# Kernel tuning notes

Hardware: AMD Instinct MI355X
Metric: run time of the kernel (lower is better)

The kernel has to match this reference:

```python
import jax, jax.numpy as jnp
import numpy as np

ANGLE_SCALE = 100.0
DIST_SCALE = 100.0
DIST_BOUNDARY = 0.0
HID = 128
N_HIDDEN = 2  # output_layer
EPS = 1e-08


def _mlp(x, w0, b0, ws, bs):
    # Linear, then N_HIDDEN x (ReLU, Linear)
    h = x @ w0 + b0
    for i in range(ws.shape[0]):
        h = jax.nn.relu(h) @ ws[i] + bs[i]
    return h


def _capsule_endpoints(x):
    # x: [..., 9] -> A, B endpoints of capsule segment, radius r
    c, s = jnp.cos(x[..., 3:4] * ANGLE_SCALE), jnp.sin(x[..., 3:4] * ANGLE_SCALE)
    half = x[..., 2:3] / 2
    ctr = x[..., 0:2]
    off = jnp.concatenate([half * c, half * s], axis=-1)
    return ctr - off, ctr + off, x[..., 4:5]


def _pt_seg_dist(P, A, AB, AB_sq):
    t = jnp.clip(((P - A) * AB).sum(-1, keepdims=True) / AB_sq, 0.0, 1.0)
    Q = A + t * AB
    return jnp.linalg.norm(P - Q, axis=-1, keepdims=True)


def _dist_to_capsule(init_e, query_e):
    A1, B1, r1 = _capsule_endpoints(init_e)
    A2, B2, r2 = _capsule_endpoints(query_e)
    A1B1, A2B2 = B1 - A1, B2 - A2
    s1 = (A1B1 ** 2).sum(-1, keepdims=True) + EPS
    s2 = (A2B2 ** 2).sum(-1, keepdims=True) + EPS
    d = jnp.minimum(
        jnp.minimum(_pt_seg_dist(A2, A1, A1B1, s1), _pt_seg_dist(B2, A1, A1B1, s1)),
        jnp.minimum(_pt_seg_dist(A1, A2, A2B2, s2), _pt_seg_dist(B1, A2, A2B2, s2)),
    )
    return d - r1 - r2


def setup_inputs() -> dict:
    key = jax.random.key(0)
    ks = jax.random.split(key, 32)
    B, O, T = 64, 64, 64
    f = lambda k, shp, scale=1.0: jax.random.normal(k, shp, dtype=jnp.float32) * scale
    inp = {
        'init_x': f(ks[0], (B, O, 9)),
        'query_x': f(ks[1], (B, T, 9)),
        'init_v': f(ks[2], (B, O, 2)),
        'query_v': f(ks[3], (B, T, 2)),
        'init_angular_v': f(ks[4], (B, O, 1)),
        'query_angular_v': f(ks[5], (B, T, 1)),
        'trunk_w0': f(ks[6], (9, HID), 0.3), 'trunk_b0': f(ks[7], (HID,), 0.1),
        'trunk_ws': f(ks[8], (N_HIDDEN, HID, HID), 0.08), 'trunk_bs': f(ks[9], (N_HIDDEN, HID), 0.1),
        'branch_w0': f(ks[10], (5, HID), 0.3), 'branch_b0': f(ks[11], (HID,), 0.1),
        'branch_ws': f(ks[12], (N_HIDDEN, HID, HID), 0.08), 'branch_bs': f(ks[13], (N_HIDDEN, HID), 0.1),
        'out_w': f(ks[14], (HID, 3), 0.08), 'out_b': f(ks[15], (3,), 0.1),
        'spring_w0': f(ks[16], (1, HID), 0.3), 'spring_b0': f(ks[17], (HID,), 0.1),
        'spring_w1': f(ks[18], (HID, 1), 0.08), 'spring_b1': f(ks[19], (1,), 0.1),
        'joint_w0': f(ks[20], (15, HID), 0.3), 'joint_b0': f(ks[21], (HID,), 0.1),
        'joint_w1': f(ks[22], (HID, 2), 0.08), 'joint_b1': f(ks[23], (2,), 0.1),
    }
    return inp


def reference(init_x, query_x, init_v, query_v, init_angular_v, query_angular_v,
              trunk_w0, trunk_b0, trunk_ws, trunk_bs,
              branch_w0, branch_b0, branch_ws, branch_bs,
              out_w, out_b, spring_w0, spring_b0, spring_w1, spring_b1,
              joint_w0, joint_b0, joint_w1, joint_b1):
    B, O, _ = init_x.shape
    T = query_x.shape[1]
    # pairwise broadcast: init along obj axis (dim1), query along target axis (dim2)
    init_e = jnp.broadcast_to(init_x[:, :, None, :], (B, O, T, 9))
    query_e = jnp.broadcast_to(query_x[:, None, :, :], (B, O, T, 9))
    rel = query_e[..., :2] - init_e[..., :2]
    query_e = jnp.concatenate([rel, query_e[..., 2:]], axis=-1)
    init_e = jnp.concatenate([jnp.zeros_like(rel), init_e[..., 2:]], axis=-1)
    qv = query_v[:, None, :, :] - init_v[:, :, None, :]           # [B,O,T,2]
    qav = query_angular_v[:, None, :, :] - init_angular_v[:, :, None, :]  # [B,O,T,1]
    iav = jnp.broadcast_to(init_angular_v[:, :, None, :], (B, O, T, 1))

    dist = _dist_to_capsule(init_e, query_e)
    dist_mask = (dist <= DIST_BOUNDARY).astype(jnp.float32)
    dist_input = dist * dist_mask * DIST_SCALE

    branch_in = init_e[..., :5]
    trunk_in = jnp.concatenate([query_e[..., :5], qv, qav, dist_input], axis=-1)
    branch_out = _mlp(branch_in, branch_w0, branch_b0, branch_ws, branch_bs)
    trunk_out = _mlp(trunk_in, trunk_w0, trunk_b0, trunk_ws, trunk_bs)
    force = (branch_out * trunk_out) @ out_w + out_b  # [B,O,T,3]

    # spring force
    have_spring = ((init_e[..., 8:9] == query_e[..., 8:9]) & (init_e[..., 8:9] > 0)).astype(jnp.float32)
    dvec = init_e[..., :2] - query_e[..., :2]
    length = jnp.linalg.norm(dvec, axis=-1, keepdims=True)
    dvec = dvec / (length + EPS)
    sf = jax.nn.relu(length @ spring_w0 + spring_b0) @ spring_w1 + spring_b1  # [B,O,T,1]
    sf = sf * dvec
    sf = jnp.concatenate([sf, jnp.zeros_like(sf[..., :1])], axis=-1) * have_spring

    # joint force (torch .long() truncates toward zero)
    i7, q7 = init_e[..., 7:8], query_e[..., 7:8]
    have_joint = ((jnp.trunc(i7) == jnp.trunc(q7)) & (i7 > 0)).astype(jnp.float32)
    joint_in = jnp.concatenate([init_e[..., :5], query_e[..., :5], qv, iav, qav, i7 - jnp.trunc(i7)], axis=-1)
    jf = jax.nn.relu(joint_in @ joint_w0 + joint_b0) @ joint_w1 + joint_b1  # [B,O,T,2]
    jf = jf * have_joint
    jf = jnp.concatenate([jf, jnp.zeros_like(jf[..., :1])], axis=-1)

    force = force * dist_mask + sf + jf
    return force
```

## Files before the change

kernel.cpp:

```cpp
#include <hip/hip_runtime.h>
#include <math.h>


typedef _Float16 h4v __attribute__((ext_vector_type(4)));
typedef _Float16 h8v __attribute__((ext_vector_type(8)));
typedef float    f4v __attribute__((ext_vector_type(4)));

#define AH 136

#define TW0_OFF 0
#define JW0_OFF 4096
#define TWS_OFF 8192
#define BW0_OFF 40960
#define BWS_OFF 45056
#define W_TOTAL 77824
#define BR_OFF_F (W_TOTAL/2)

#define H_ACTA 0
#define H_ACTB 8704
#define H_TINB 8704
#define H_JINB 10752
#define SMH_SIZE 17408

#define F_SCAL  0
#define SMF_SIZE 384

#define FRAG_BLOCKS 304
#define BR_BLOCKS   256

__global__ __launch_bounds__(256)
void prep_kernel(const float* __restrict__ tw0, const float* __restrict__ tws,
                 const float* __restrict__ jw0, const float* __restrict__ bw0,
                 const float* __restrict__ bws, const float* __restrict__ bb0,
                 const float* __restrict__ bbs, const float* __restrict__ init_x,
                 _Float16* __restrict__ wsH, float* __restrict__ brw)
{
    __shared__ float bsm[2*16*132];
    const int tid = threadIdx.x;

    if (blockIdx.x < FRAG_BLOCKS) {
        int idx = blockIdx.x * 256 + tid;
        if (idx >= W_TOTAL) return;
        const int j = idx & 7;
        const int lane = (idx >> 3) & 63;
        const int q = lane >> 4, r = lane & 15;
        _Float16 v;
        if (idx < JW0_OFF) {
            int mt = idx >> 9;
            int k = q*8 + j, m = mt*16 + r;
            v = (k < 9) ? (_Float16)tw0[k*128 + m] : (_Float16)0.f;
        } else if (idx < TWS_OFF) {
            int mt = (idx - JW0_OFF) >> 9;
            int k = q*8 + j, m = mt*16 + r;
            v = (k < 15) ? (_Float16)jw0[k*128 + m] : (_Float16)0.f;
        } else if (idx < BW0_OFF) {
            int e = idx - TWS_OFF;
            int ks = (e >> 9) & 3, mt = (e >> 11) & 7, l = e >> 14;
            int k = ks*32 + q*8 + j, m = mt*16 + r;
            v = (_Float16)tws[l*16384 + k*128 + m];
        } else if (idx < BWS_OFF) {
            int mt = (idx - BW0_OFF) >> 9;
            int k = q*8 + j, m = mt*16 + r;
            v = (k < 5) ? (_Float16)bw0[k*128 + m] : (_Float16)0.f;
        } else {
            int e = idx - BWS_OFF;
            int ks = (e >> 9) & 3, mt = (e >> 11) & 7, l = e >> 14;
            int k = ks*32 + q*8 + j, m = mt*16 + r;
            v = (_Float16)bws[l*16384 + k*128 + m];
        }
        wsH[idx] = v;
        return;
    }

    const int blk2 = blockIdx.x - FRAG_BLOCKS;
    const int row0 = blk2*16;
    const int lane = tid & 63, w = tid >> 6;
    const int q = lane >> 4, r = lane & 15;
    float* h0 = bsm;
    float* h1 = bsm + 16*132;

    for (int e = tid; e < 2048; e += 256) {
        const int rw = e >> 7, n = e & 127;
        const float* ixp = init_x + (row0 + rw)*9;
        float acc = bb0[n];
        acc = fmaf(ixp[2], bw0[2*128 + n], acc);
        acc = fmaf(ixp[3], bw0[3*128 + n], acc);
        acc = fmaf(ixp[4], bw0[4*128 + n], acc);
        h0[rw*132 + n] = acc;
    }
    __syncthreads();

    #pragma unroll
    for (int L = 0; L < 2; ++L) {
        const float* Wg = bws + L*16384;
        const float* bi = bbs + L*128;
        const float* in = (L == 0) ? h0 : h1;
        #pragma unroll
        for (int mi = 0; mi < 2; ++mi) {
            const int mt = w + mi*4;
            const int m0 = mt*16 + q*4;
            h8v af[4];
            #pragma unroll
            for (int ks = 0; ks < 4; ++ks)
                #pragma unroll
                for (int j = 0; j < 8; ++j)
                    af[ks][j] = (_Float16)Wg[(ks*32 + q*8 + j)*128 + mt*16 + r];
            f4v acc = *(const f4v*)&bi[m0];
            #pragma unroll
            for (int ks = 0; ks < 4; ++ks) {
                f4v x0 = *(const f4v*)&in[r*132 + ks*32 + q*8];
                f4v x1 = *(const f4v*)&in[r*132 + ks*32 + q*8 + 4];
                h8v bf;
                #pragma unroll
                for (int i = 0; i < 4; ++i) {
                    bf[i]   = (_Float16)fmaxf(x0[i], 0.f);
                    bf[4+i] = (_Float16)fmaxf(x1[i], 0.f);
                }
                acc = __builtin_amdgcn_mfma_f32_16x16x32_f16(af[ks], bf, acc, 0, 0, 0);
            }
            if (L == 0)
                *(f4v*)&h1[r*132 + m0] = acc;
            else
                *(f4v*)&brw[(row0 + r)*128 + m0] = acc;
        }
        __syncthreads();
    }
}

__device__ __forceinline__ void layerK32_rw(const h8v af,
        const float* __restrict__ bias, const _Float16* __restrict__ inB,
        _Float16* __restrict__ actOut, int lane, int mtg)
{
    const int q = lane >> 4, r = lane & 15;
    #pragma unroll
    for (int nt = 0; nt < 4; ++nt) {
        h8v bf = *(const h8v*)&inB[(nt*64 + lane)*8];
        f4v acc = *(const f4v*)&bias[mtg*16 + q*4];
        acc = __builtin_amdgcn_mfma_f32_16x16x32_f16(af, bf, acc, 0, 0, 0);
        h4v o;
        #pragma unroll
        for (int i = 0; i < 4; ++i) o[i] = (_Float16)fmaxf(acc[i], 0.f);
        *(h4v*)&actOut[(nt*16 + r)*AH + mtg*16 + q*4] = o;
    }
}

__device__ __forceinline__ void layerK128_rw(const h8v af[4],
        const float* __restrict__ bias, const _Float16* __restrict__ actIn,
        _Float16* __restrict__ actOut, int lane, int mtg)
{
    const int q = lane >> 4, r = lane & 15;
    #pragma unroll
    for (int nt = 0; nt < 4; ++nt) {
        h8v bf[4];
        #pragma unroll
        for (int ks = 0; ks < 4; ++ks)
            bf[ks] = *(const h8v*)&actIn[(nt*16 + r)*AH + ks*32 + q*8];
        f4v acc = *(const f4v*)&bias[mtg*16 + q*4];
        #pragma unroll
        for (int ks = 0; ks < 4; ++ks)
            acc = __builtin_amdgcn_mfma_f32_16x16x32_f16(af[ks], bf[ks], acc, 0, 0, 0);
        h4v o;
        #pragma unroll
        for (int i = 0; i < 4; ++i) o[i] = (_Float16)fmaxf(acc[i], 0.f);
        *(h4v*)&actOut[(nt*16 + r)*AH + mtg*16 + q*4] = o;
    }
}

__device__ __forceinline__ void layerK128_regs_rw(const h8v af[4],
        const float* __restrict__ bias, const _Float16* __restrict__ actIn,
        f4v accT[4], int lane, int mtg)
{
    const int q = lane >> 4, r = lane & 15;
    #pragma unroll
    for (int nt = 0; nt < 4; ++nt) {
        h8v bf[4];
        #pragma unroll
        for (int ks = 0; ks < 4; ++ks)
            bf[ks] = *(const h8v*)&actIn[(nt*16 + r)*AH + ks*32 + q*8];
        f4v acc = *(const f4v*)&bias[mtg*16 + q*4];
        #pragma unroll
        for (int ks = 0; ks < 4; ++ks)
            acc = __builtin_amdgcn_mfma_f32_16x16x32_f16(af[ks], bf[ks], acc, 0, 0, 0);
        accT[nt] = acc;
    }
}

__global__ __launch_bounds__(512, 4)
void ff_kernel(const float* __restrict__ init_x,  const float* __restrict__ query_x,
               const float* __restrict__ init_v,  const float* __restrict__ query_v,
               const float* __restrict__ init_av, const float* __restrict__ query_av,
               const float* __restrict__ tb0, const float* __restrict__ tbs,
               const float* __restrict__ out_w, const float* __restrict__ out_b,
               const float* __restrict__ sw0, const float* __restrict__ sb0,
               const float* __restrict__ sw1, const float* __restrict__ sb1,
               const float* __restrict__ jb0,
               const float* __restrict__ jw1, const float* __restrict__ jb1,
               const _Float16* __restrict__ wsH, const float* __restrict__ brw,
               float* __restrict__ out)
{
    __shared__ __align__(16) _Float16 smh[SMH_SIZE];
    __shared__ float smf[SMF_SIZE];
    float* const fred = (float*)smh;
    const int tid = threadIdx.x;
    const int bid = blockIdx.x;
    const int o  = bid & 63;
    const int b  = bid >> 6;
    const int lane = tid & 63, w = tid >> 6;
    const int q = lane >> 4, r = lane & 15;
    const float* ix = init_x + (b*64 + o)*9;

    h8v afT0 = *(const h8v*)&wsH[TW0_OFF + (w*64 + lane)*8];
    h8v afJ0 = *(const h8v*)&wsH[JW0_OFF + (w*64 + lane)*8];
    f4v br   = *(const f4v*)&brw[bid*128 + w*16 + q*4];

    {
        const int rq   = lane & 7;
        const int cand = (lane >> 3) & 3;
        const int tq   = w*8 + rq;
        const float* qx = query_x + (b*64 + tq)*9;
        const float ix0 = ix[0], ix1 = ix[1], ix2 = ix[2], ix3 = ix[3], ix4 = ix[4];
        const float ix7 = ix[7], ix8 = ix[8];
        const float qx0 = qx[0], qx1 = qx[1], qx2 = qx[2], qx3 = qx[3], qx4 = qx[4];
        const float qx7 = qx[7], qx8 = qx[8];
        const float rel0 = qx0 - ix0, rel1 = qx1 - ix1;

        float s1v, c1v; sincosf(ix3 * 100.f, &s1v, &c1v);
        float s2v, c2v; sincosf(qx3 * 100.f, &s2v, &c2v);
        const float h1 = ix2 * 0.5f, h2 = qx2 * 0.5f;
        const float o1x = h1*c1v, o1y = h1*s1v;
        const float o2x = h2*c2v, o2y = h2*s2v;
        const float A1x = -o1x, A1y = -o1y;
        const float A2x = rel0 - o2x, A2y = rel1 - o2y;
        const float B2x = rel0 + o2x, B2y = rel1 + o2y;
        const float ab1x = 2.f*o1x, ab1y = 2.f*o1y;
        const float ab2x = 2.f*o2x, ab2y = 2.f*o2y;
        const float s1sq = ab1x*ab1x + ab1y*ab1y + 1e-8f;
        const float s2sq = ab2x*ab2x + ab2y*ab2y + 1e-8f;

        float Px, Py, Ax, Ay, ABx, ABy, ss;
        if (cand < 2) {
            Ax = A1x; Ay = A1y; ABx = ab1x; ABy = ab1y; ss = s1sq;
            Px = (cand == 0) ? A2x : B2x;  Py = (cand == 0) ? A2y : B2y;
        } else {
            Ax = A2x; Ay = A2y; ABx = ab2x; ABy = ab2y; ss = s2sq;
            Px = (cand == 2) ? A1x : o1x;  Py = (cand == 2) ? A1y : o1y;
        }
        float t = ((Px - Ax)*ABx + (Py - Ay)*ABy) / ss;
        t = fminf(fmaxf(t, 0.f), 1.f);
        const float dx = Px - (Ax + t*ABx);
        const float dy = Py - (Ay + t*ABy);
        float dq = sqrtf(dx*dx + dy*dy);
        dq = fminf(dq, __shfl_xor(dq, 8));
        dq = fminf(dq, __shfl_xor(dq, 16));

        if ((lane & 56) == 0) {
            const float dist = dq - ix4 - qx4;
            const float mask = (dist <= 0.f) ? 1.f : 0.f;
            const float dinp = dist * mask * 100.f;
            const float qv0 = query_v[(b*64+tq)*2+0] - init_v[(b*64+o)*2+0];
            const float qv1 = query_v[(b*64+tq)*2+1] - init_v[(b*64+o)*2+1];
            const float iav = init_av[b*64+o];
            const float qav = query_av[b*64+tq] - iav;

            const int fb = (tq >> 4)*512 + (tq & 15)*8;
            h8v t0, t1 = {}, z = {};
            t0[0]=(_Float16)rel0; t0[1]=(_Float16)rel1; t0[2]=(_Float16)qx2;
            t0[3]=(_Float16)qx3;  t0[4]=(_Float16)qx4;  t0[5]=(_Float16)qv0;
            t0[6]=(_Float16)qv1;  t0[7]=(_Float16)qav;
            t1[0]=(_Float16)dinp;
            *(h8v*)&smh[H_TINB + fb]       = t0;
            *(h8v*)&smh[H_TINB + fb + 128] = t1;
            *(h8v*)&smh[H_TINB + fb + 256] = z;
            *(h8v*)&smh[H_TINB + fb + 384] = z;
            h8v j0, j1 = {};
            j0[0]=(_Float16)0.f;  j0[1]=(_Float16)0.f;  j0[2]=(_Float16)ix2;
            j0[3]=(_Float16)ix3;  j0[4]=(_Float16)ix4;  j0[5]=(_Float16)rel0;
            j0[6]=(_Float16)rel1; j0[7]=(_Float16)qx2;
            j1[0]=(_Float16)qx3;  j1[1]=(_Float16)qx4;  j1[2]=(_Float16)qv0;
            j1[3]=(_Float16)qv1;  j1[4]=(_Float16)iav;  j1[5]=(_Float16)qav;
            j1[6]=(_Float16)(ix7 - truncf(ix7));
            *(h8v*)&smh[H_JINB + fb]       = j0;
            *(h8v*)&smh[H_JINB + fb + 128] = j1;
            *(h8v*)&smh[H_JINB + fb + 256] = z;
            *(h8v*)&smh[H_JINB + fb + 384] = z;

            const float len = sqrtf(rel0*rel0 + rel1*rel1);
            const float inv = 1.f / (len + 1e-8f);
            smf[F_SCAL +       tq] = mask;
            smf[F_SCAL +  64 + tq] = len;
            smf[F_SCAL + 128 + tq] = -rel0 * inv;
            smf[F_SCAL + 192 + tq] = -rel1 * inv;
            smf[F_SCAL + 256 + tq] = ((ix8 == qx8) && (ix8 > 0.f)) ? 1.f : 0.f;
            smf[F_SCAL + 320 + tq] = ((truncf(ix7) == truncf(qx7)) && (ix7 > 0.f)) ? 1.f : 0.f;
        }
    }
    __syncthreads();

    h8v afT1[4];
    #pragma unroll
    for (int ks = 0; ks < 4; ++ks)
        afT1[ks] = *(const h8v*)&wsH[TWS_OFF + ((w*4 + ks)*64 + lane)*8];

    float jf0[4] = {0,0,0,0}, jf1[4] = {0,0,0,0};
    layerK32_rw(afT0, tb0, smh + H_TINB, smh + H_ACTA, lane, w);
    {
        const int m0 = w*16 + q*4;
        f4v bv  = *(const f4v*)&jb0[m0];
        f4v jwa = *(const f4v*)&jw1[m0*2];
        f4v jwb = *(const f4v*)&jw1[m0*2 + 4];
        #pragma unroll
        for (int nt = 0; nt < 4; ++nt) {
            h8v bf = *(const h8v*)&smh[H_JINB + (nt*64 + lane)*8];
            f4v a = bv;
            a = __builtin_amdgcn_mfma_f32_16x16x32_f16(afJ0, bf, a, 0, 0, 0);
            float jw[8] = {jwa[0], jwa[1], jwa[2], jwa[3],
                           jwb[0], jwb[1], jwb[2], jwb[3]};
            #pragma unroll
            for (int i = 0; i < 4; ++i) {
                const float jh = fmaxf(a[i], 0.f);
                jf0[nt] = fmaf(jh, jw[i*2+0], jf0[nt]);
                jf1[nt] = fmaf(jh, jw[i*2+1], jf1[nt]);
            }
        }
    }
    __syncthreads();

    h8v afT2[4];
    #pragma unroll
    for (int ks = 0; ks < 4; ++ks)
        afT2[ks] = *(const h8v*)&wsH[TWS_OFF + 16384 + ((w*4 + ks)*64 + lane)*8];

    layerK128_rw(afT1, tbs, smh + H_ACTA, smh + H_ACTB, lane, w);
    __syncthreads();

    f4v accT[4];
    layerK128_regs_rw(afT2, tbs + 128, smh + H_ACTB, accT, lane, w);

    float f0[4] = {0,0,0,0}, f1[4] = {0,0,0,0}, f2[4] = {0,0,0,0};
    float sp[4] = {0,0,0,0};

    {
        const int m0 = w*16 + q*4;
        f4v oa = *(const f4v*)&out_w[m0*3];
        f4v ob = *(const f4v*)&out_w[m0*3 + 4];
        f4v oc = *(const f4v*)&out_w[m0*3 + 8];
        float ow[12] = {oa[0],oa[1],oa[2],oa[3], ob[0],ob[1],ob[2],ob[3],
                        oc[0],oc[1],oc[2],oc[3]};
        #pragma unroll
        for (int nt = 0; nt < 4; ++nt)
            #pragma unroll
            for (int i = 0; i < 4; ++i) {
                const float prod = accT[nt][i] * br[i];
                f0[nt] = fmaf(prod, ow[i*3+0], f0[nt]);
                f1[nt] = fmaf(prod, ow[i*3+1], f1[nt]);
                f2[nt] = fmaf(prod, ow[i*3+2], f2[nt]);
            }
    }
    {
        float lenv[4];
        #pragma unroll
        for (int nt = 0; nt < 4; ++nt) lenv[nt] = smf[F_SCAL + 64 + nt*16 + r];
        const int m0 = w*16 + q*4;
        f4v w0v = *(const f4v*)&sw0[m0];
        f4v b0v = *(const f4v*)&sb0[m0];
        f4v w1v = *(const f4v*)&sw1[m0];
        #pragma unroll
        for (int i = 0; i < 4; ++i)
            #pragma unroll
            for (int nt = 0; nt < 4; ++nt) {
                const float sv = fmaxf(fmaf(lenv[nt], w0v[i], b0v[i]), 0.f);
                sp[nt] = fmaf(sv, w1v[i], sp[nt]);
            }
    }
    #pragma unroll
    for (int nt = 0; nt < 4; ++nt) {
        float v[6] = {f0[nt], f1[nt], f2[nt], jf0[nt], jf1[nt], sp[nt]};
        #pragma unroll
        for (int k = 0; k < 6; ++k) {
            v[k] += __shfl_xor(v[k], 16);
            v[k] += __shfl_xor(v[k], 32);
        }
        if (lane < 16) {
            float* rd = &fred[(w*64 + nt*16 + r)*7];
            rd[0]=v[0]; rd[1]=v[1]; rd[2]=v[2]; rd[3]=v[3]; rd[4]=v[4]; rd[5]=v[5];
        }
    }
    __syncthreads();

    if (tid < 64) {
        const int t = tid;
        float s0=0.f, s1=0.f, s2=0.f, s3=0.f, s4=0.f, s5=0.f;
        #pragma unroll
        for (int ww = 0; ww < 8; ++ww) {
            const float* rd = &fred[(ww*64 + t)*7];
            s0 += rd[0]; s1 += rd[1]; s2 += rd[2];
            s3 += rd[3]; s4 += rd[4]; s5 += rd[5];
        }
        const float mask = smf[F_SCAL + t];
        const float dvx  = smf[F_SCAL + 128 + t];
        const float dvy  = smf[F_SCAL + 192 + t];
        const float hs   = smf[F_SCAL + 256 + t];
        const float hj   = smf[F_SCAL + 320 + t];
        const float sf = (s5 + sb1[0]) * hs;
        const float j0 = (s3 + jb1[0]) * hj;
        const float j1 = (s4 + jb1[1]) * hj;
        float* op = out + (((b*64 + o)*64) + t)*3;
        op[0] = (s0 + out_b[0])*mask + sf*dvx + j0;
        op[1] = (s1 + out_b[1])*mask + sf*dvy + j1;
        op[2] = (s2 + out_b[2])*mask;
    }
}

extern "C" void kernel_launch(void* const* d_in, const int* in_sizes, int n_in,
                              void* d_out, int out_size, void* d_ws, size_t ws_size,
                              hipStream_t stream) {
    (void)in_sizes; (void)n_in; (void)out_size; (void)ws_size;
    _Float16* wsH = (_Float16*)d_ws;
    float* brw = (float*)d_ws + BR_OFF_F;

    prep_kernel<<<dim3(FRAG_BLOCKS + BR_BLOCKS), dim3(256), 0, stream>>>(
        (const float*)d_in[6],
        (const float*)d_in[8],
        (const float*)d_in[20],
        (const float*)d_in[10],
        (const float*)d_in[12],
        (const float*)d_in[11],
        (const float*)d_in[13],
        (const float*)d_in[0],
        wsH, brw);
    ff_kernel<<<dim3(64*64), dim3(512), 0, stream>>>(
        (const float*)d_in[0],  (const float*)d_in[1],  (const float*)d_in[2],
        (const float*)d_in[3],  (const float*)d_in[4],  (const float*)d_in[5],
        (const float*)d_in[7],  (const float*)d_in[9],
        (const float*)d_in[14], (const float*)d_in[15],
        (const float*)d_in[16], (const float*)d_in[17],
        (const float*)d_in[18], (const float*)d_in[19],
        (const float*)d_in[21],
        (const float*)d_in[22], (const float*)d_in[23],
        wsH, brw, (float*)d_out);
}
```

Before: 166.2 us.

## Compute each (b,o) tile in a single wavefront with register-resident activations

The main kernel moves from 512-thread blocks (8 waves, each owning 16 hidden units and sharing activations through LDS with barriers) to one 64-lane wave per (b,o) that computes all 128 hidden units itself. Activations between MLP layers stay in registers as packed fp16 and are reshuffled into MFMA B-fragment layout with cross-lane shuffles. This removes LDS traffic, __syncthreads and the cross-wave reduction. In exchange each wave does 8x the MFMA work serially, reloads weight fragments from global/L2 per tile, and has much higher register pressure, which may limit occupancy.

```diff
diff --git a/kernel.cpp b/kernel.cpp
--- a/kernel.cpp
+++ b/kernel.cpp
@@ -5,8 +5,7 @@
 typedef _Float16 h4v __attribute__((ext_vector_type(4)));
 typedef _Float16 h8v __attribute__((ext_vector_type(8)));
 typedef float    f4v __attribute__((ext_vector_type(4)));
-
-#define AH 136
+typedef unsigned int u32;
 
 #define TW0_OFF 0
 #define JW0_OFF 4096
@@ -15,15 +14,6 @@
 #define BWS_OFF 45056
 #define W_TOTAL 77824
 #define BR_OFF_F (W_TOTAL/2)
-
-#define H_ACTA 0
-#define H_ACTB 8704
-#define H_TINB 8704
-#define H_JINB 10752
-#define SMH_SIZE 17408
-
-#define F_SCAL  0
-#define SMF_SIZE 384
 
 #define FRAG_BLOCKS 304
 #define BR_BLOCKS   256
@@ -127,65 +117,38 @@
     }
 }
 
-__device__ __forceinline__ void layerK32_rw(const h8v af,
-        const float* __restrict__ bias, const _Float16* __restrict__ inB,
-        _Float16* __restrict__ actOut, int lane, int mtg)
-{
-    const int q = lane >> 4, r = lane & 15;
-    #pragma unroll
-    for (int nt = 0; nt < 4; ++nt) {
-        h8v bf = *(const h8v*)&inB[(nt*64 + lane)*8];
-        f4v acc = *(const f4v*)&bias[mtg*16 + q*4];
-        acc = __builtin_amdgcn_mfma_f32_16x16x32_f16(af, bf, acc, 0, 0, 0);
-        h4v o;
-        #pragma unroll
-        for (int i = 0; i < 4; ++i) o[i] = (_Float16)fmaxf(acc[i], 0.f);
-        *(h4v*)&actOut[(nt*16 + r)*AH + mtg*16 + q*4] = o;
-    }
-}
-
-__device__ __forceinline__ void layerK128_rw(const h8v af[4],
-        const float* __restrict__ bias, const _Float16* __restrict__ actIn,
-        _Float16* __restrict__ actOut, int lane, int mtg)
-{
-    const int q = lane >> 4, r = lane & 15;
-    #pragma unroll
-    for (int nt = 0; nt < 4; ++nt) {
-        h8v bf[4];
-        #pragma unroll
-        for (int ks = 0; ks < 4; ++ks)
-            bf[ks] = *(const h8v*)&actIn[(nt*16 + r)*AH + ks*32 + q*8];
-        f4v acc = *(const f4v*)&bias[mtg*16 + q*4];
-        #pragma unroll
-        for (int ks = 0; ks < 4; ++ks)
-            acc = __builtin_amdgcn_mfma_f32_16x16x32_f16(af[ks], bf[ks], acc, 0, 0, 0);
-        h4v o;
-        #pragma unroll
-        for (int i = 0; i < 4; ++i) o[i] = (_Float16)fmaxf(acc[i], 0.f);
-        *(h4v*)&actOut[(nt*16 + r)*AH + mtg*16 + q*4] = o;
-    }
-}
-
-__device__ __forceinline__ void layerK128_regs_rw(const h8v af[4],
-        const float* __restrict__ bias, const _Float16* __restrict__ actIn,
-        f4v accT[4], int lane, int mtg)
-{
-    const int q = lane >> 4, r = lane & 15;
-    #pragma unroll
-    for (int nt = 0; nt < 4; ++nt) {
-        h8v bf[4];
-        #pragma unroll
-        for (int ks = 0; ks < 4; ++ks)
-            bf[ks] = *(const h8v*)&actIn[(nt*16 + r)*AH + ks*32 + q*8];
-        f4v acc = *(const f4v*)&bias[mtg*16 + q*4];
-        #pragma unroll
-        for (int ks = 0; ks < 4; ++ks)
-            acc = __builtin_amdgcn_mfma_f32_16x16x32_f16(af[ks], bf[ks], acc, 0, 0, 0);
-        accT[nt] = acc;
-    }
-}
-
-__global__ __launch_bounds__(512, 4)
+__device__ __forceinline__ u32 sh_u32(u32 v, int idx) {
+    return (u32)__shfl((int)v, idx, 64);
+}
+__device__ __forceinline__ h8v make_h8(u32 a, u32 b, u32 c, u32 d) {
+    union { u32 u[4]; h8v h; } t;
+    t.u[0] = a; t.u[1] = b; t.u[2] = c; t.u[3] = d;
+    return t.h;
+}
+__device__ __forceinline__ u32 pack_relu2(float x, float y) {
+    union { _Float16 h[2]; u32 u; } t;
+    t.h[0] = (_Float16)fmaxf(x, 0.f);
+    t.h[1] = (_Float16)fmaxf(y, 0.f);
+    return t.u;
+}
+
+#define BUILD_BF(dst, P) do {                                                 \
+    _Pragma("unroll")                                                         \
+    for (int ks_ = 0; ks_ < 4; ++ks_) {                                       \
+        u32 lo0 = sh_u32((P)[2*ks_][0],   idxA);                              \
+        u32 hi0 = sh_u32((P)[2*ks_+1][0], idxA);                              \
+        u32 lo1 = sh_u32((P)[2*ks_][1],   idxA);                              \
+        u32 hi1 = sh_u32((P)[2*ks_+1][1], idxA);                              \
+        u32 lo2 = sh_u32((P)[2*ks_][0],   idxB);                              \
+        u32 hi2 = sh_u32((P)[2*ks_+1][0], idxB);                              \
+        u32 lo3 = sh_u32((P)[2*ks_][1],   idxB);                              \
+        u32 hi3 = sh_u32((P)[2*ks_+1][1], idxB);                              \
+        (dst)[ks_] = make_h8(hiSel ? hi0 : lo0, hiSel ? hi1 : lo1,            \
+                             hiSel ? hi2 : lo2, hiSel ? hi3 : lo3);           \
+    }                                                                         \
+} while (0)
+
+__global__ __launch_bounds__(64)
 void ff_kernel(const float* __restrict__ init_x,  const float* __restrict__ query_x,
                const float* __restrict__ init_v,  const float* __restrict__ query_v,
                const float* __restrict__ init_av, const float* __restrict__ query_av,
@@ -198,216 +161,220 @@
                const _Float16* __restrict__ wsH, const float* __restrict__ brw,
                float* __restrict__ out)
 {
-    __shared__ __align__(16) _Float16 smh[SMH_SIZE];
-    __shared__ float smf[SMF_SIZE];
-    float* const fred = (float*)smh;
-    const int tid = threadIdx.x;
-    const int bid = blockIdx.x;
-    const int o  = bid & 63;
-    const int b  = bid >> 6;
-    const int lane = tid & 63, w = tid >> 6;
-    const int q = lane >> 4, r = lane & 15;
-    const float* ix = init_x + (b*64 + o)*9;
-
-    h8v afT0 = *(const h8v*)&wsH[TW0_OFF + (w*64 + lane)*8];
-    h8v afJ0 = *(const h8v*)&wsH[JW0_OFF + (w*64 + lane)*8];
-    f4v br   = *(const f4v*)&brw[bid*128 + w*16 + q*4];
-
-    {
-        const int rq   = lane & 7;
-        const int cand = (lane >> 3) & 3;
-        const int tq   = w*8 + rq;
+    const int lane = threadIdx.x;
+    const int bid  = blockIdx.x;
+    const int b    = bid >> 6;
+    const int g    = lane >> 4, c = lane & 15;
+    const int idxA = (g & 1)*32 + c;
+    const int idxB = idxA + 16;
+    const bool hiSel = (lane & 32) != 0;
+
+    const float* ix = init_x + bid*9;
+    const float ix0 = ix[0], ix1 = ix[1], ix2 = ix[2], ix3 = ix[3], ix4 = ix[4];
+    const float ix7 = ix[7], ix8 = ix[8];
+    float s1v, c1v; sincosf(ix3 * 100.f, &s1v, &c1v);
+    const float hh1 = ix2 * 0.5f;
+    const float o1x = hh1*c1v, o1y = hh1*s1v;
+    const float A1x = -o1x, A1y = -o1y;
+    const float ab1x = 2.f*o1x, ab1y = 2.f*o1y;
+    const float s1sq = ab1x*ab1x + ab1y*ab1y + 1e-8f;
+    const float iv0 = init_v[bid*2+0], iv1 = init_v[bid*2+1];
+    const float iav = init_av[bid];
+    const float i7t = truncf(ix7);
+    const float fr7 = ix7 - i7t;
+
+    u32  p[4][8][2];
+    float mask_[4], dvx_[4], dvy_[4], hs_[4], hj_[4], len_[4];
+    float jf0_[4], jf1_[4];
+
+    #pragma unroll
+    for (int nt = 0; nt < 4; ++nt) {
+        const int tq = nt*16 + c;
         const float* qx = query_x + (b*64 + tq)*9;
-        const float ix0 = ix[0], ix1 = ix[1], ix2 = ix[2], ix3 = ix[3], ix4 = ix[4];
-        const float ix7 = ix[7], ix8 = ix[8];
         const float qx0 = qx[0], qx1 = qx[1], qx2 = qx[2], qx3 = qx[3], qx4 = qx[4];
         const float qx7 = qx[7], qx8 = qx[8];
         const float rel0 = qx0 - ix0, rel1 = qx1 - ix1;
 
-        float s1v, c1v; sincosf(ix3 * 100.f, &s1v, &c1v);
         float s2v, c2v; sincosf(qx3 * 100.f, &s2v, &c2v);
-        const float h1 = ix2 * 0.5f, h2 = qx2 * 0.5f;
-        const float o1x = h1*c1v, o1y = h1*s1v;
-        const float o2x = h2*c2v, o2y = h2*s2v;
-        const float A1x = -o1x, A1y = -o1y;
+        const float hh2 = qx2 * 0.5f;
+        const float o2x = hh2*c2v, o2y = hh2*s2v;
         const float A2x = rel0 - o2x, A2y = rel1 - o2y;
         const float B2x = rel0 + o2x, B2y = rel1 + o2y;
-        const float ab1x = 2.f*o1x, ab1y = 2.f*o1y;
         const float ab2x = 2.f*o2x, ab2y = 2.f*o2y;
-        const float s1sq = ab1x*ab1x + ab1y*ab1y + 1e-8f;
         const float s2sq = ab2x*ab2x + ab2y*ab2y + 1e-8f;
 
         float Px, Py, Ax, Ay, ABx, ABy, ss;
-        if (cand < 2) {
+        if (g < 2) {
             Ax = A1x; Ay = A1y; ABx = ab1x; ABy = ab1y; ss = s1sq;
-            Px = (cand == 0) ? A2x : B2x;  Py = (cand == 0) ? A2y : B2y;
+            Px = (g == 0) ? A2x : B2x;  Py = (g == 0) ? A2y : B2y;
         } else {
             Ax = A2x; Ay = A2y; ABx = ab2x; ABy = ab2y; ss = s2sq;
-            Px = (cand == 2) ? A1x : o1x;  Py = (cand == 2) ? A1y : o1y;
+            Px = (g == 2) ? A1x : o1x;  Py = (g == 2) ? A1y : o1y;
         }
         float t = ((Px - Ax)*ABx + (Py - Ay)*ABy) / ss;
         t = fminf(fmaxf(t, 0.f), 1.f);
         const float dx = Px - (Ax + t*ABx);
         const float dy = Py - (Ay + t*ABy);
         float dq = sqrtf(dx*dx + dy*dy);
-        dq = fminf(dq, __shfl_xor(dq, 8));
         dq = fminf(dq, __shfl_xor(dq, 16));
-
-        if ((lane & 56) == 0) {
-            const float dist = dq - ix4 - qx4;
-            const float mask = (dist <= 0.f) ? 1.f : 0.f;
-            const float dinp = dist * mask * 100.f;
-            const float qv0 = query_v[(b*64+tq)*2+0] - init_v[(b*64+o)*2+0];
-            const float qv1 = query_v[(b*64+tq)*2+1] - init_v[(b*64+o)*2+1];
-            const float iav = init_av[b*64+o];
-            const float qav = query_av[b*64+tq] - iav;
-
-            const int fb = (tq >> 4)*512 + (tq & 15)*8;
-            h8v t0, t1 = {}, z = {};
-            t0[0]=(_Float16)rel0; t0[1]=(_Float16)rel1; t0[2]=(_Float16)qx2;
-            t0[3]=(_Float16)qx3;  t0[4]=(_Float16)qx4;  t0[5]=(_Float16)qv0;
-            t0[6]=(_Float16)qv1;  t0[7]=(_Float16)qav;
-            t1[0]=(_Float16)dinp;
-            *(h8v*)&smh[H_TINB + fb]       = t0;
-            *(h8v*)&smh[H_TINB + fb + 128] = t1;
-            *(h8v*)&smh[H_TINB + fb + 256] = z;
-            *(h8v*)&smh[H_TINB + fb + 384] = z;
-            h8v j0, j1 = {};
-            j0[0]=(_Float16)0.f;  j0[1]=(_Float16)0.f;  j0[2]=(_Float16)ix2;
-            j0[3]=(_Float16)ix3;  j0[4]=(_Float16)ix4;  j0[5]=(_Float16)rel0;
-            j0[6]=(_Float16)rel1; j0[7]=(_Float16)qx2;
-            j1[0]=(_Float16)qx3;  j1[1]=(_Float16)qx4;  j1[2]=(_Float16)qv0;
-            j1[3]=(_Float16)qv1;  j1[4]=(_Float16)iav;  j1[5]=(_Float16)qav;
-            j1[6]=(_Float16)(ix7 - truncf(ix7));
-            *(h8v*)&smh[H_JINB + fb]       = j0;
-            *(h8v*)&smh[H_JINB + fb + 128] = j1;
-            *(h8v*)&smh[H_JINB + fb + 256] = z;
-            *(h8v*)&smh[H_JINB + fb + 384] = z;
-
-            const float len = sqrtf(rel0*rel0 + rel1*rel1);
-            const float inv = 1.f / (len + 1e-8f);
-            smf[F_SCAL +       tq] = mask;
-            smf[F_SCAL +  64 + tq] = len;
-            smf[F_SCAL + 128 + tq] = -rel0 * inv;
-            smf[F_SCAL + 192 + tq] = -rel1 * inv;
-            smf[F_SCAL + 256 + tq] = ((ix8 == qx8) && (ix8 > 0.f)) ? 1.f : 0.f;
-            smf[F_SCAL + 320 + tq] = ((truncf(ix7) == truncf(qx7)) && (ix7 > 0.f)) ? 1.f : 0.f;
-        }
-    }
-    __syncthreads();
-
-    h8v afT1[4];
-    #pragma unroll
-    for (int ks = 0; ks < 4; ++ks)
-        afT1[ks] = *(const h8v*)&wsH[TWS_OFF + ((w*4 + ks)*64 + lane)*8];
-
-    float jf0[4] = {0,0,0,0}, jf1[4] = {0,0,0,0};
-    layerK32_rw(afT0, tb0, smh + H_TINB, smh + H_ACTA, lane, w);
-    {
-        const int m0 = w*16 + q*4;
-        f4v bv  = *(const f4v*)&jb0[m0];
-        f4v jwa = *(const f4v*)&jw1[m0*2];
-        f4v jwb = *(const f4v*)&jw1[m0*2 + 4];
-        #pragma unroll
-        for (int nt = 0; nt < 4; ++nt) {
-            h8v bf = *(const h8v*)&smh[H_JINB + (nt*64 + lane)*8];
-            f4v a = bv;
-            a = __builtin_amdgcn_mfma_f32_16x16x32_f16(afJ0, bf, a, 0, 0, 0);
-            float jw[8] = {jwa[0], jwa[1], jwa[2], jwa[3],
-                           jwb[0], jwb[1], jwb[2], jwb[3]};
-            #pragma unroll
-            for (int i = 0; i < 4; ++i) {
-                const float jh = fmaxf(a[i], 0.f);
-                jf0[nt] = fmaf(jh, jw[i*2+0], jf0[nt]);
-                jf1[nt] = fmaf(jh, jw[i*2+1], jf1[nt]);
-            }
-        }
-    }
-    __syncthreads();
-
-    h8v afT2[4];
-    #pragma unroll
-    for (int ks = 0; ks < 4; ++ks)
-        afT2[ks] = *(const h8v*)&wsH[TWS_OFF + 16384 + ((w*4 + ks)*64 + lane)*8];
-
-    layerK128_rw(afT1, tbs, smh + H_ACTA, smh + H_ACTB, lane, w);
-    __syncthreads();
-
-    f4v accT[4];
-    layerK128_regs_rw(afT2, tbs + 128, smh + H_ACTB, accT, lane, w);
-
-    float f0[4] = {0,0,0,0}, f1[4] = {0,0,0,0}, f2[4] = {0,0,0,0};
-    float sp[4] = {0,0,0,0};
-
-    {
-        const int m0 = w*16 + q*4;
-        f4v oa = *(const f4v*)&out_w[m0*3];
-        f4v ob = *(const f4v*)&out_w[m0*3 + 4];
-        f4v oc = *(const f4v*)&out_w[m0*3 + 8];
-        float ow[12] = {oa[0],oa[1],oa[2],oa[3], ob[0],ob[1],ob[2],ob[3],
-                        oc[0],oc[1],oc[2],oc[3]};
-        #pragma unroll
-        for (int nt = 0; nt < 4; ++nt)
-            #pragma unroll
-            for (int i = 0; i < 4; ++i) {
-                const float prod = accT[nt][i] * br[i];
-                f0[nt] = fmaf(prod, ow[i*3+0], f0[nt]);
-                f1[nt] = fmaf(prod, ow[i*3+1], f1[nt]);
-                f2[nt] = fmaf(prod, ow[i*3+2], f2[nt]);
-            }
-    }
-    {
-        float lenv[4];
-        #pragma unroll
-        for (int nt = 0; nt < 4; ++nt) lenv[nt] = smf[F_SCAL + 64 + nt*16 + r];
-        const int m0 = w*16 + q*4;
-        f4v w0v = *(const f4v*)&sw0[m0];
-        f4v b0v = *(const f4v*)&sb0[m0];
-        f4v w1v = *(const f4v*)&sw1[m0];
+        dq = fminf(dq, __shfl_xor(dq, 32));
+
+        const float dist = dq - ix4 - qx4;
+        const float mask = (dist <= 0.f) ? 1.f : 0.f;
+        const float dinp = dist * mask * 100.f;
+        const float qv0 = query_v[(b*64+tq)*2+0] - iv0;
+        const float qv1 = query_v[(b*64+tq)*2+1] - iv1;
+        const float qav = query_av[b*64+tq] - iav;
+        const float len = sqrtf(rel0*rel0 + rel1*rel1);
+        const float inv = 1.f / (len + 1e-8f);
+
+        mask_[nt] = mask;
+        dvx_[nt]  = -rel0 * inv;
+        dvy_[nt]  = -rel1 * inv;
+        hs_[nt]   = ((ix8 == qx8) && (ix8 > 0.f)) ? 1.f : 0.f;
+        hj_[nt]   = ((i7t == truncf(qx7)) && (ix7 > 0.f)) ? 1.f : 0.f;
+        len_[nt]  = len;
+
+        const bool g0 = (g == 0), g1 = (g == 1);
+        h8v bT, bJ;
+        bT[0] = (_Float16)(g0 ? rel0 : g1 ? dinp : 0.f);
+        bT[1] = (_Float16)(g0 ? rel1 : 0.f);
+        bT[2] = (_Float16)(g0 ? qx2  : 0.f);
+        bT[3] = (_Float16)(g0 ? qx3  : 0.f);
+        bT[4] = (_Float16)(g0 ? qx4  : 0.f);
+        bT[5] = (_Float16)(g0 ? qv0  : 0.f);
+        bT[6] = (_Float16)(g0 ? qv1  : 0.f);
+        bT[7] = (_Float16)(g0 ? qav  : 0.f);
+        bJ[0] = (_Float16)(g1 ? qx3  : 0.f);
+        bJ[1] = (_Float16)(g1 ? qx4  : 0.f);
+        bJ[2] = (_Float16)(g0 ? ix2  : g1 ? qv0 : 0.f);
+        bJ[3] = (_Float16)(g0 ? ix3  : g1 ? qv1 : 0.f);
+        bJ[4] = (_Float16)(g0 ? ix4  : g1 ? iav : 0.f);
+        bJ[5] = (_Float16)(g0 ? rel0 : g1 ? qav : 0.f);
+        bJ[6] = (_Float16)(g0 ? rel1 : g1 ? fr7 : 0.f);
+        bJ[7] = (_Float16)(g0 ? qx2  : 0.f);
+
+        float jf0 = 0.f, jf1 = 0.f;
+        #pragma unroll
+        for (int mt = 0; mt < 8; ++mt) {
+            const int m0 = mt*16 + g*4;
+            h8v aT = *(const h8v*)&wsH[TW0_OFF + (mt*64 + lane)*8];
+            f4v accT = *(const f4v*)&tb0[m0];
+            accT = __builtin_amdgcn_mfma_f32_16x16x32_f16(aT, bT, accT, 0, 0, 0);
+            p[nt][mt][0] = pack_relu2(accT[0], accT[1]);
+            p[nt][mt][1] = pack_relu2(accT[2], accT[3]);
+
+            h8v aJ = *(const h8v*)&wsH[JW0_OFF + (mt*64 + lane)*8];
+            f4v accJ = *(const f4v*)&jb0[m0];
+            accJ = __builtin_amdgcn_mfma_f32_16x16x32_f16(aJ, bJ, accJ, 0, 0, 0);
+            f4v jwa = *(const f4v*)&jw1[m0*2];
+            f4v jwb = *(const f4v*)&jw1[m0*2 + 4];
+            const float h0r = fmaxf(accJ[0], 0.f), h1r = fmaxf(accJ[1], 0.f);
+            const float h2r = fmaxf(accJ[2], 0.f), h3r = fmaxf(accJ[3], 0.f);
+            jf0 = fmaf(h0r, jwa[0], fmaf(h1r, jwa[2], fmaf(h2r, jwb[0], fmaf(h3r, jwb[2], jf0))));
+            jf1 = fmaf(h0r, jwa[1], fmaf(h1r, jwa[3], fmaf(h2r, jwb[1], fmaf(h3r, jwb[3], jf1))));
+        }
+        jf0_[nt] = jf0; jf1_[nt] = jf1;
+    }
+
+    float sp_[4] = {0.f, 0.f, 0.f, 0.f};
+    #pragma unroll
+    for (int ch = 0; ch < 8; ++ch) {
+        const int n0 = g*32 + ch*4;
+        f4v w0v = *(const f4v*)&sw0[n0];
+        f4v b0v = *(const f4v*)&sb0[n0];
+        f4v w1v = *(const f4v*)&sw1[n0];
         #pragma unroll
         for (int i = 0; i < 4; ++i)
             #pragma unroll
-            for (int nt = 0; nt < 4; ++nt) {
-                const float sv = fmaxf(fmaf(lenv[nt], w0v[i], b0v[i]), 0.f);
-                sp[nt] = fmaf(sv, w1v[i], sp[nt]);
+            for (int nt = 0; nt < 4; ++nt)
+                sp_[nt] = fmaf(fmaxf(fmaf(len_[nt], w0v[i], b0v[i]), 0.f), w1v[i], sp_[nt]);
+    }
+
+    #pragma unroll
+    for (int prn = 0; prn < 2; ++prn) {
+        h8v bf[2][4];
+        #pragma unroll
+        for (int n2 = 0; n2 < 2; ++n2)
+            BUILD_BF(bf[n2], p[prn*2 + n2]);
+        #pragma unroll
+        for (int mt = 0; mt < 8; ++mt) {
+            const int m0 = mt*16 + g*4;
+            h8v a0 = *(const h8v*)&wsH[TWS_OFF + ((mt*4 + 0)*64 + lane)*8];
+            h8v a1 = *(const h8v*)&wsH[TWS_OFF + ((mt*4 + 1)*64 + lane)*8];
+            h8v a2 = *(const h8v*)&wsH[TWS_OFF + ((mt*4 + 2)*64 + lane)*8];
+            h8v a3 = *(const h8v*)&wsH[TWS_OFF + ((mt*4 + 3)*64 + lane)*8];
+            f4v bias = *(const f4v*)&tbs[m0];
+            #pragma unroll
+            for (int n2 = 0; n2 < 2; ++n2) {
+                f4v acc = bias;
+                acc = __builtin_amdgcn_mfma_f32_16x16x32_f16(a0, bf[n2][0], acc, 0, 0, 0);
+                acc = __builtin_amdgcn_mfma_f32_16x16x32_f16(a1, bf[n2][1], acc, 0, 0, 0);
+                acc = __builtin_amdgcn_mfma_f32_16x16x32_f16(a2, bf[n2][2], acc, 0, 0, 0);
+                acc = __builtin_amdgcn_mfma_f32_16x16x32_f16(a3, bf[n2][3], acc, 0, 0, 0);
+                p[prn*2 + n2][mt][0] = pack_relu2(acc[0], acc[1]);
+                p[prn*2 + n2][mt][1] = pack_relu2(acc[2], acc[3]);
             }
-    }
+        }
+    }
+
+    float f0_[4] = {0,0,0,0}, f1_[4] = {0,0,0,0}, f2_[4] = {0,0,0,0};
+    #pragma unroll
+    for (int prn = 0; prn < 2; ++prn) {
+        h8v bf[2][4];
+        #pragma unroll
+        for (int n2 = 0; n2 < 2; ++n2)
+            BUILD_BF(bf[n2], p[prn*2 + n2]);
+        #pragma unroll
+        for (int mt = 0; mt < 8; ++mt) {
+            const int m0 = mt*16 + g*4;
+            h8v a0 = *(const h8v*)&wsH[TWS_OFF + 16384 + ((mt*4 + 0)*64 + lane)*8];
+            h8v a1 = *(const h8v*)&wsH[TWS_OFF + 16384 + ((mt*4 + 1)*64 + lane)*8];
+            h8v a2 = *(const h8v*)&wsH[TWS_OFF + 16384 + ((mt*4 + 2)*64 + lane)*8];
+            h8v a3 = *(const h8v*)&wsH[TWS_OFF + 16384 + ((mt*4 + 3)*64 + lane)*8];
+            f4v bias = *(const f4v*)&tbs[128 + m0];
+            f4v brv  = *(const f4v*)&brw[bid*128 + m0];
+            f4v oa = *(const f4v*)&out_w[m0*3];
+            f4v ob = *(const f4v*)&out_w[m0*3 + 4];
+            f4v oc = *(const f4v*)&out_w[m0*3 + 8];
+            #pragma unroll
+            for (int n2 = 0; n2 < 2; ++n2) {
+                const int nt = prn*2 + n2;
+                f4v acc = bias;
+                acc = __builtin_amdgcn_mfma_f32_16x16x32_f16(a0, bf[n2][0], acc, 0, 0, 0);
+                acc = __builtin_amdgcn_mfma_f32_16x16x32_f16(a1, bf[n2][1], acc, 0, 0, 0);
+                acc = __builtin_amdgcn_mfma_f32_16x16x32_f16(a2, bf[n2][2], acc, 0, 0, 0);
+                acc = __builtin_amdgcn_mfma_f32_16x16x32_f16(a3, bf[n2][3], acc, 0, 0, 0);
+                const float pr0 = acc[0]*brv[0], pr1 = acc[1]*brv[1];
+                const float pr2 = acc[2]*brv[2], pr3 = acc[3]*brv[3];
+                f0_[nt] += pr0*oa[0] + pr1*oa[3] + pr2*ob[2] + pr3*oc[1];
+                f1_[nt] += pr0*oa[1] + pr1*ob[0] + pr2*ob[3] + pr3*oc[2];
+                f2_[nt] += pr0*oa[2] + pr1*ob[1] + pr2*oc[0] + pr3*oc[3];
+            }
+        }
+    }
+
+    const float obs0 = out_b[0], obs1 = out_b[1], obs2 = out_b[2];
+    const float sb1v = sb1[0], jb1a = jb1[0], jb1b = jb1[1];
     #pragma unroll
     for (int nt = 0; nt < 4; ++nt) {
-        float v[6] = {f0[nt], f1[nt], f2[nt], jf0[nt], jf1[nt], sp[nt]};
-        #pragma unroll
-        for (int k = 0; k < 6; ++k) {
-            v[k] += __shfl_xor(v[k], 16);
-            v[k] += __shfl_xor(v[k], 32);
-        }
-        if (lane < 16) {
-            float* rd = &fred[(w*64 + nt*16 + r)*7];
-            rd[0]=v[0]; rd[1]=v[1]; rd[2]=v[2]; rd[3]=v[3]; rd[4]=v[4]; rd[5]=v[5];
-        }
-    }
-    __syncthreads();
-
-    if (tid < 64) {
-        const int t = tid;
-        float s0=0.f, s1=0.f, s2=0.f, s3=0.f, s4=0.f, s5=0.f;
-        #pragma unroll
-        for (int ww = 0; ww < 8; ++ww) {
-            const float* rd = &fred[(ww*64 + t)*7];
-            s0 += rd[0]; s1 += rd[1]; s2 += rd[2];
-            s3 += rd[3]; s4 += rd[4]; s5 += rd[5];
-        }
-        const float mask = smf[F_SCAL + t];
-        const float dvx  = smf[F_SCAL + 128 + t];
-        const float dvy  = smf[F_SCAL + 192 + t];
-        const float hs   = smf[F_SCAL + 256 + t];
-        const float hj   = smf[F_SCAL + 320 + t];
-        const float sf = (s5 + sb1[0]) * hs;
-        const float j0 = (s3 + jb1[0]) * hj;
-        const float j1 = (s4 + jb1[1]) * hj;
-        float* op = out + (((b*64 + o)*64) + t)*3;
-        op[0] = (s0 + out_b[0])*mask + sf*dvx + j0;
-        op[1] = (s1 + out_b[1])*mask + sf*dvy + j1;
-        op[2] = (s2 + out_b[2])*mask;
+        float v0 = f0_[nt], v1 = f1_[nt], v2 = f2_[nt];
+        float v3 = jf0_[nt], v4 = jf1_[nt], v5 = sp_[nt];
+        v0 += __shfl_xor(v0, 16); v0 += __shfl_xor(v0, 32);
+        v1 += __shfl_xor(v1, 16); v1 += __shfl_xor(v1, 32);
+        v2 += __shfl_xor(v2, 16); v2 += __shfl_xor(v2, 32);
+        v3 += __shfl_xor(v3, 16); v3 += __shfl_xor(v3, 32);
+        v4 += __shfl_xor(v4, 16); v4 += __shfl_xor(v4, 32);
+        v5 += __shfl_xor(v5, 16); v5 += __shfl_xor(v5, 32);
+        if (g == 0) {
+            const float sf = (v5 + sb1v) * hs_[nt];
+            const float j0 = (v3 + jb1a) * hj_[nt];
+            const float j1 = (v4 + jb1b) * hj_[nt];
+            float* op = out + (bid*64 + nt*16 + c)*3;
+            op[0] = (v0 + obs0)*mask_[nt] + sf*dvx_[nt] + j0;
+            op[1] = (v1 + obs1)*mask_[nt] + sf*dvy_[nt] + j1;
+            op[2] = (v2 + obs2)*mask_[nt];
+        }
     }
 }
 
@@ -428,7 +395,7 @@
         (const float*)d_in[13],
         (const float*)d_in[0],
         wsH, brw);
-    ff_kernel<<<dim3(64*64), dim3(512), 0, stream>>>(
+    ff_kernel<<<dim3(64*64), dim3(64), 0, stream>>>(
         (const float*)d_in[0],  (const float*)d_in[1],  (const float*)d_in[2],
         (const float*)d_in[3],  (const float*)d_in[4],  (const float*)d_in[5],
         (const float*)d_in[7],  (const float*)d_in[9],
```

New measurement: 266.7 us. 1.6x slower.
